# Kernel tuning notes

Measured on AMD Instinct MI355X. Metric: run time of the kernel, lower is better.

The kernel has to match this reference:

```python
import jax, jax.numpy as jnp
import numpy as np

N = 100000
E = 1600000
DIN = 128
HID = 128
EPS = 1e-5


def setup_inputs() -> dict:
    key = jax.random.key(0)
    ks = jax.random.split(key, 16)
    s = lambda i, shape, sc=0.05: jax.random.normal(ks[i], shape, dtype=jnp.float32) * sc
    inp = {
        "x": jax.random.normal(ks[0], (N, DIN), dtype=jnp.float32),
        "edge_index": jax.random.randint(ks[1], (2, E), 0, N, dtype=jnp.int64),
        # layer 1
        "W1": s(2, (DIN, HID)), "b1": jnp.zeros((HID,), jnp.float32),
        "g1": jnp.ones((HID,), jnp.float32), "be1": jnp.zeros((HID,), jnp.float32),
        "m1": s(3, (HID,)), "v1": jax.random.uniform(ks[4], (HID,), jnp.float32) + 0.5,
        # layer 2
        "W2": s(5, (HID, HID)), "b2": jnp.zeros((HID,), jnp.float32),
        "g2": jnp.ones((HID,), jnp.float32), "be2": jnp.zeros((HID,), jnp.float32),
        "m2": s(6, (HID,)), "v2": jax.random.uniform(ks[7], (HID,), jnp.float32) + 0.5,
        # classifier
        "Wc1": s(8, (HID, HID // 2)), "bc1": jnp.zeros((HID // 2,), jnp.float32),
        "Wc2": s(9, (HID // 2, 2)), "bc2": jnp.zeros((2,), jnp.float32),
    }
    return inp


def _gnn_layer(x, W, b, src, dst):
    # linear then scatter-mean of source features onto destinations
    h = x @ W + b                                    # [N, HID]
    msg_sum = jax.ops.segment_sum(h[src], dst, num_segments=N)   # [N, HID]
    cnt = jax.ops.segment_sum(jnp.ones((src.shape[0],), h.dtype), dst, num_segments=N)
    return msg_sum / cnt[:, None]                    # self-loops guarantee cnt >= 1


def _bn(x, g, be, m, v):
    return (x - m) * jax.lax.rsqrt(v + EPS) * g + be


def reference(x, edge_index, W1, b1, g1, be1, m1, v1, W2, b2, g2, be2, m2, v2, Wc1, bc1, Wc2, bc2):
    # add self loops (PyG add_self_loops appends [i, i])
    loop = jnp.arange(N, dtype=edge_index.dtype)
    src = jnp.concatenate([edge_index[0], loop])
    dst = jnp.concatenate([edge_index[1], loop])

    h = _gnn_layer(x, W1, b1, src, dst)
    h = jax.nn.relu(_bn(h, g1, be1, m1, v1))
    h = _gnn_layer(h, W2, b2, src, dst)
    h = jax.nn.relu(_bn(h, g2, be2, m2, v2))

    h = jax.nn.relu(h @ Wc1 + bc1)
    return h @ Wc2 + bc2                              # logits [N, 2]
```

## Files before the change

### kernel.cpp

```cpp
#include <hip/hip_runtime.h>
#include <hip/hip_bf16.h>

#define EPS 1e-5f

using bf16x8 = __attribute__((ext_vector_type(8))) short;
using f32x4  = __attribute__((ext_vector_type(4))) float;

__device__ __forceinline__ void bf16_split(float f, unsigned short& h, unsigned short& l) {
    unsigned u = __float_as_uint(f);
    unsigned hu = (u + 0x8000u) & 0xFFFF0000u;
    float fh = __uint_as_float(hu);
    h = (unsigned short)(hu >> 16);
    float rl = f - fh;
    unsigned ul = __float_as_uint(rl);
    l = (unsigned short)((ul + 0x8000u) >> 16);
}

__global__ __launch_bounds__(256) void k_wprep(const float* __restrict__ W1,
                                               const float* __restrict__ W2,
                                               unsigned short* __restrict__ w1h,
                                               unsigned short* __restrict__ w1l,
                                               unsigned short* __restrict__ w2h,
                                               unsigned short* __restrict__ w2l) {
    int idx = blockIdx.x * 256 + threadIdx.x;
    if (idx >= 32768) return;
    int mtx = idx >> 14;
    int rem = idx & 16383;
    int k = rem >> 7, n = rem & 127;
    float w = mtx ? W2[k * 128 + n] : W1[k * 128 + n];
    unsigned short h, l;
    bf16_split(w, h, l);
    if (mtx) { w2h[n * 128 + k] = h; w2l[n * 128 + k] = l; }
    else     { w1h[n * 128 + k] = h; w1l[n * 128 + k] = l; }
}

__global__ __launch_bounds__(256) void k_histrank(const int* __restrict__ dst,
                                                  int* __restrict__ counts,
                                                  int* __restrict__ rank, int nE) {
    int i = blockIdx.x * 256 + threadIdx.x;
    if (i < nE) {
        int p = atomicAdd(&counts[dst[i]], 1);
        __builtin_nontemporal_store(p, &rank[i]);
    }
}

__global__ __launch_bounds__(256) void k_scan1(const int* __restrict__ counts,
                                               int* __restrict__ bsums, int n) {
    __shared__ int sdata[256];
    int base = blockIdx.x * 2048;
    int t = threadIdx.x;
    int s = 0;
#pragma unroll
    for (int i = 0; i < 8; ++i) {
        int idx = base + t * 8 + i;
        if (idx < n) s += counts[idx];
    }
    sdata[t] = s;
    __syncthreads();
    for (int off = 128; off > 0; off >>= 1) {
        if (t < off) sdata[t] += sdata[t + off];
        __syncthreads();
    }
    if (t == 0) bsums[blockIdx.x] = sdata[0];
}

__global__ __launch_bounds__(64) void k_scan2(int* __restrict__ bsums, int nb) {
    if (threadIdx.x == 0 && blockIdx.x == 0) {
        int acc = 0;
        for (int i = 0; i < nb; ++i) { int v = bsums[i]; bsums[i] = acc; acc += v; }
    }
}

__global__ __launch_bounds__(256) void k_scan3(const int* __restrict__ counts,
                                               const int* __restrict__ bsums,
                                               int* __restrict__ rowstart,
                                               int n, int nE) {
    __shared__ int sth[256];
    int base = blockIdx.x * 2048;
    int t = threadIdx.x;
    int loc[8];
    int s = 0;
#pragma unroll
    for (int i = 0; i < 8; ++i) {
        int idx = base + t * 8 + i;
        loc[i] = s;
        s += (idx < n) ? counts[idx] : 0;
    }
    sth[t] = s;
    __syncthreads();
    for (int off = 1; off < 256; off <<= 1) {
        int tmp = (t >= off) ? sth[t - off] : 0;
        __syncthreads();
        sth[t] += tmp;
        __syncthreads();
    }
    int excl = sth[t] - s + bsums[blockIdx.x];
#pragma unroll
    for (int i = 0; i < 8; ++i) {
        int idx = base + t * 8 + i;
        if (idx < n) rowstart[idx] = excl + loc[i];
    }
    if (blockIdx.x == 0 && t == 0) rowstart[n] = nE;
}

__global__ __launch_bounds__(256) void k_fill3(const int* __restrict__ srci,
                                               const int* __restrict__ dsti,
                                               const int* __restrict__ rank,
                                               const int* __restrict__ rowstart,
                                               int* __restrict__ col, int nE) {
    int e = blockIdx.x * 256 + threadIdx.x;
    if (e < nE) {
        col[rowstart[dsti[e]] + rank[e]] = srci[e];
    }
}

__global__ __launch_bounds__(256) void k_linmf(const float* __restrict__ X,
                                               const unsigned short* __restrict__ WhT,
                                               const unsigned short* __restrict__ WlT,
                                               const float* __restrict__ bias,
                                               float* __restrict__ out, int nRows) {
    __shared__ __align__(16) unsigned short xh[64][136];
    __shared__ __align__(16) unsigned short xl[64][136];
    int row0 = blockIdx.x * 64;
    int tid = threadIdx.x;

    for (int i = tid; i < 64 * 32; i += 256) {
        int r = i >> 5, c4 = (i & 31) << 2;
        float4 v = make_float4(0.f, 0.f, 0.f, 0.f);
        int row = row0 + r;
        if (row < nRows) v = *(const float4*)(X + (size_t)row * 128 + c4);
        unsigned short h0, l0, h1, l1, h2, l2, h3, l3;
        bf16_split(v.x, h0, l0); bf16_split(v.y, h1, l1);
        bf16_split(v.z, h2, l2); bf16_split(v.w, h3, l3);
        xh[r][c4] = h0; xh[r][c4 + 1] = h1; xh[r][c4 + 2] = h2; xh[r][c4 + 3] = h3;
        xl[r][c4] = l0; xl[r][c4 + 1] = l1; xl[r][c4 + 2] = l2; xl[r][c4 + 3] = l3;
    }
    __syncthreads();

    int w = tid >> 6, lane = tid & 63;
    int t16 = lane & 15;
    int kg = lane >> 4;

    f32x4 acc[8];
#pragma unroll
    for (int ct = 0; ct < 8; ++ct) acc[ct] = (f32x4){0.f, 0.f, 0.f, 0.f};

    for (int k0 = 0; k0 < 128; k0 += 32) {
        bf16x8 ah = *(const bf16x8*)&xh[w * 16 + t16][k0 + kg * 8];
        bf16x8 al = *(const bf16x8*)&xl[w * 16 + t16][k0 + kg * 8];
#pragma unroll
        for (int ct = 0; ct < 8; ++ct) {
            size_t boff = (size_t)(ct * 16 + t16) * 128 + k0 + kg * 8;
            bf16x8 bh = *(const bf16x8*)(WhT + boff);
            bf16x8 bl = *(const bf16x8*)(WlT + boff);
            acc[ct] = __builtin_amdgcn_mfma_f32_16x16x32_bf16(ah, bh, acc[ct], 0, 0, 0);
            acc[ct] = __builtin_amdgcn_mfma_f32_16x16x32_bf16(ah, bl, acc[ct], 0, 0, 0);
            acc[ct] = __builtin_amdgcn_mfma_f32_16x16x32_bf16(al, bh, acc[ct], 0, 0, 0);
        }
    }

#pragma unroll
    for (int ct = 0; ct < 8; ++ct) {
        int c = ct * 16 + t16;
        float b = bias[c];
#pragma unroll
        for (int j = 0; j < 4; ++j) {
            int r = row0 + w * 16 + kg * 4 + j;
            if (r < nRows) out[(size_t)r * 128 + c] = acc[ct][j] + b;
        }
    }
}

template <bool FUSE_BN>
__global__ __launch_bounds__(256) void k_gather(const float* __restrict__ src,
                                                const int* __restrict__ rowstart,
                                                const int* __restrict__ col,
                                                const float* __restrict__ g,
                                                const float* __restrict__ be,
                                                const float* __restrict__ m,
                                                const float* __restrict__ v,
                                                float* __restrict__ out, int nRows) {
    int r = blockIdx.x * 4 + (threadIdx.x >> 6);
    if (r >= nRows) return;
    int lane = threadIdx.x & 63;
    int half = lane >> 5;
    int li = lane & 31;
    int d0 = li * 4;
    int s = rowstart[r], e = rowstart[r + 1];
    int deg = e - s;

    float4 acc = make_float4(0.f, 0.f, 0.f, 0.f);
    if (half == 0) acc = *(const float4*)(src + (size_t)r * 128 + d0);

    int nP = deg >> 1;
    int p = 0;
    for (; p + 4 <= nP; p += 4) {
        int jb = s + 2 * p + half;
        int c0i = col[jb], c1i = col[jb + 2], c2i = col[jb + 4], c3i = col[jb + 6];
        float4 t0 = *(const float4*)(src + (size_t)c0i * 128 + d0);
        float4 t1 = *(const float4*)(src + (size_t)c1i * 128 + d0);
        float4 t2 = *(const float4*)(src + (size_t)c2i * 128 + d0);
        float4 t3 = *(const float4*)(src + (size_t)c3i * 128 + d0);
        acc.x += (t0.x + t1.x) + (t2.x + t3.x);
        acc.y += (t0.y + t1.y) + (t2.y + t3.y);
        acc.z += (t0.z + t1.z) + (t2.z + t3.z);
        acc.w += (t0.w + t1.w) + (t2.w + t3.w);
    }
    for (; p < nP; ++p) {
        int ci = col[s + 2 * p + half];
        float4 t = *(const float4*)(src + (size_t)ci * 128 + d0);
        acc.x += t.x; acc.y += t.y; acc.z += t.z; acc.w += t.w;
    }
    if ((deg & 1) && half == 0) {
        int ci = col[e - 1];
        float4 t = *(const float4*)(src + (size_t)ci * 128 + d0);
        acc.x += t.x; acc.y += t.y; acc.z += t.z; acc.w += t.w;
    }

    acc.x += __shfl_xor(acc.x, 32, 64);
    acc.y += __shfl_xor(acc.y, 32, 64);
    acc.z += __shfl_xor(acc.z, 32, 64);
    acc.w += __shfl_xor(acc.w, 32, 64);

    if (half == 0) {
        float rc = 1.0f / (float)(deg + 1);
        float4 o;
        if (FUSE_BN) {
            float4 gv  = *(const float4*)(g + d0);
            float4 bev = *(const float4*)(be + d0);
            float4 mv  = *(const float4*)(m + d0);
            float4 vv  = *(const float4*)(v + d0);
            o.x = fmaxf((acc.x * rc - mv.x) * rsqrtf(vv.x + EPS) * gv.x + bev.x, 0.f);
            o.y = fmaxf((acc.y * rc - mv.y) * rsqrtf(vv.y + EPS) * gv.y + bev.y, 0.f);
            o.z = fmaxf((acc.z * rc - mv.z) * rsqrtf(vv.z + EPS) * gv.z + bev.z, 0.f);
            o.w = fmaxf((acc.w * rc - mv.w) * rsqrtf(vv.w + EPS) * gv.w + bev.w, 0.f);
        } else {
            o.x = acc.x * rc; o.y = acc.y * rc; o.z = acc.z * rc; o.w = acc.w * rc;
        }
        *(float4*)(out + (size_t)r * 128 + d0) = o;
    }
}

__global__ __launch_bounds__(256) void k_final(const float* __restrict__ xin,
                                               const float* __restrict__ Wc1,
                                               const float* __restrict__ bc1,
                                               const float* __restrict__ Wc2,
                                               const float* __restrict__ bc2,
                                               float* __restrict__ out, int nRows) {
    __shared__ float xs[32][132];
    __shared__ float w1s[128][64];
    __shared__ float hs[32][68];
    int row0 = blockIdx.x * 32;
    int tid = threadIdx.x;

    for (int i = tid; i < 2048; i += 256) {
        int kk = i >> 4, c4 = (i & 15) << 2;
        *(float4*)&w1s[kk][c4] = *(const float4*)(Wc1 + kk * 64 + c4);
    }
    for (int i = tid; i < 1024; i += 256) {
        int r = i >> 5, c4 = (i & 31) << 2;
        int row = row0 + r;
        float4 o = make_float4(0.f, 0.f, 0.f, 0.f);
        if (row < nRows) o = *(const float4*)(xin + (size_t)row * 128 + c4);
        *(float4*)&xs[r][c4] = o;
    }
    __syncthreads();

    int cg = tid & 15, rg = tid >> 4;
    int c0 = cg * 4, r0 = rg * 2;
    float acc[2][4];
    float4 bc = *(const float4*)(bc1 + c0);
    acc[0][0] = bc.x; acc[0][1] = bc.y; acc[0][2] = bc.z; acc[0][3] = bc.w;
    acc[1][0] = bc.x; acc[1][1] = bc.y; acc[1][2] = bc.z; acc[1][3] = bc.w;
    for (int k = 0; k < 128; ++k) {
        float4 w4 = *(const float4*)&w1s[k][c0];
        float x0 = xs[r0][k], x1 = xs[r0 + 1][k];
        acc[0][0] = fmaf(x0, w4.x, acc[0][0]);
        acc[0][1] = fmaf(x0, w4.y, acc[0][1]);
        acc[0][2] = fmaf(x0, w4.z, acc[0][2]);
        acc[0][3] = fmaf(x0, w4.w, acc[0][3]);
        acc[1][0] = fmaf(x1, w4.x, acc[1][0]);
        acc[1][1] = fmaf(x1, w4.y, acc[1][1]);
        acc[1][2] = fmaf(x1, w4.z, acc[1][2]);
        acc[1][3] = fmaf(x1, w4.w, acc[1][3]);
    }
    *(float4*)&hs[r0][c0] = make_float4(fmaxf(acc[0][0], 0.f), fmaxf(acc[0][1], 0.f),
                                        fmaxf(acc[0][2], 0.f), fmaxf(acc[0][3], 0.f));
    *(float4*)&hs[r0 + 1][c0] = make_float4(fmaxf(acc[1][0], 0.f), fmaxf(acc[1][1], 0.f),
                                            fmaxf(acc[1][2], 0.f), fmaxf(acc[1][3], 0.f));
    __syncthreads();

    if (tid < 64) {
        int r = tid >> 1, oc = tid & 1;
        float s = bc2[oc];
        for (int c = 0; c < 64; ++c) s = fmaf(hs[r][c], Wc2[c * 2 + oc], s);
        int row = row0 + r;
        if (row < nRows) out[(size_t)row * 2 + oc] = s;
    }
}

extern "C" void kernel_launch(void* const* d_in, const int* in_sizes, int n_in,
                              void* d_out, int out_size, void* d_ws, size_t ws_size,
                              hipStream_t stream) {
    const float* x   = (const float*)d_in[0];
    const int*   ei  = (const int*)d_in[1];
    const float* W1  = (const float*)d_in[2];
    const float* b1  = (const float*)d_in[3];
    const float* g1  = (const float*)d_in[4];
    const float* be1 = (const float*)d_in[5];
    const float* m1  = (const float*)d_in[6];
    const float* v1  = (const float*)d_in[7];
    const float* W2  = (const float*)d_in[8];
    const float* b2  = (const float*)d_in[9];
    const float* g2  = (const float*)d_in[10];
    const float* be2 = (const float*)d_in[11];
    const float* m2  = (const float*)d_in[12];
    const float* v2  = (const float*)d_in[13];
    const float* Wc1 = (const float*)d_in[14];
    const float* bc1 = (const float*)d_in[15];
    const float* Wc2 = (const float*)d_in[16];
    const float* bc2 = (const float*)d_in[17];

    const int N_ = in_sizes[0] / 128;
    const int E_ = in_sizes[1] / 2;
    const int* srci = ei;
    const int* dsti = ei + E_;

    float* A = (float*)d_ws;
    float* B = A + (size_t)N_ * 128;
    int* rank = (int*)B;
    int* counts   = (int*)(B + (size_t)N_ * 128);
    int* rowstart = counts + N_;
    int* bsums    = rowstart + N_ + 1;
    int* col      = bsums + 256;
    uintptr_t wp  = ((uintptr_t)(col + E_) + 63) & ~(uintptr_t)63;
    unsigned short* w1h = (unsigned short*)wp;
    unsigned short* w1l = w1h + 16384;
    unsigned short* w2h = w1l + 16384;
    unsigned short* w2l = w2h + 16384;

    const int nb = (N_ + 2047) / 2048;

    k_wprep<<<128, 256, 0, stream>>>(W1, W2, w1h, w1l, w2h, w2l);

    hipMemsetAsync(counts, 0, (size_t)N_ * sizeof(int), stream);
    k_histrank<<<(E_ + 255) / 256, 256, 0, stream>>>(dsti, counts, rank, E_);
    k_scan1   <<<nb, 256, 0, stream>>>(counts, bsums, N_);
    k_scan2   <<<1, 64, 0, stream>>>(bsums, nb);
    k_scan3   <<<nb, 256, 0, stream>>>(counts, bsums, rowstart, N_, E_);
    k_fill3   <<<(E_ + 255) / 256, 256, 0, stream>>>(srci, dsti, rank, rowstart,
                                                     col, E_);

    k_linmf<<<(N_ + 63) / 64, 256, 0, stream>>>(x, w1h, w1l, b1, A, N_);
    k_gather<true><<<(N_ + 3) / 4, 256, 0, stream>>>(A, rowstart, col,
                                                     g1, be1, m1, v1, B, N_);

    k_linmf<<<(N_ + 63) / 64, 256, 0, stream>>>(B, w2h, w2l, b2, A, N_);
    k_gather<true><<<(N_ + 3) / 4, 256, 0, stream>>>(A, rowstart, col,
                                                     g2, be2, m2, v2, B, N_);

    k_final<<<(N_ + 31) / 32, 256, 0, stream>>>(B, Wc1, bc1, Wc2, bc2,
                                                (float*)d_out, N_);
}
```

Baseline: 652.4 us.

## Aggregate before linear and fuse layer-2 linear with classifier head

Uses linearity of mean aggregation to gather raw features first and then apply the linear layer, with bias, BN and ReLU fused into the MFMA epilogue. The second layer's linear, BN and ReLU are fused with the two-layer classifier head in one kernel that keeps the hidden tile in shared memory. This drops one full N×128 write and read plus a kernel launch. The cost is a heavier head kernel that reads Wc1 from global memory instead of staging it in LDS, and an extra shared-memory round trip.

```diff
diff --git a/kernel.cpp b/kernel.cpp
--- a/kernel.cpp
+++ b/kernel.cpp
@@ -114,71 +114,9 @@
     }
 }
 
-__global__ __launch_bounds__(256) void k_linmf(const float* __restrict__ X,
-                                               const unsigned short* __restrict__ WhT,
-                                               const unsigned short* __restrict__ WlT,
-                                               const float* __restrict__ bias,
-                                               float* __restrict__ out, int nRows) {
-    __shared__ __align__(16) unsigned short xh[64][136];
-    __shared__ __align__(16) unsigned short xl[64][136];
-    int row0 = blockIdx.x * 64;
-    int tid = threadIdx.x;
-
-    for (int i = tid; i < 64 * 32; i += 256) {
-        int r = i >> 5, c4 = (i & 31) << 2;
-        float4 v = make_float4(0.f, 0.f, 0.f, 0.f);
-        int row = row0 + r;
-        if (row < nRows) v = *(const float4*)(X + (size_t)row * 128 + c4);
-        unsigned short h0, l0, h1, l1, h2, l2, h3, l3;
-        bf16_split(v.x, h0, l0); bf16_split(v.y, h1, l1);
-        bf16_split(v.z, h2, l2); bf16_split(v.w, h3, l3);
-        xh[r][c4] = h0; xh[r][c4 + 1] = h1; xh[r][c4 + 2] = h2; xh[r][c4 + 3] = h3;
-        xl[r][c4] = l0; xl[r][c4 + 1] = l1; xl[r][c4 + 2] = l2; xl[r][c4 + 3] = l3;
-    }
-    __syncthreads();
-
-    int w = tid >> 6, lane = tid & 63;
-    int t16 = lane & 15;
-    int kg = lane >> 4;
-
-    f32x4 acc[8];
-#pragma unroll
-    for (int ct = 0; ct < 8; ++ct) acc[ct] = (f32x4){0.f, 0.f, 0.f, 0.f};
-
-    for (int k0 = 0; k0 < 128; k0 += 32) {
-        bf16x8 ah = *(const bf16x8*)&xh[w * 16 + t16][k0 + kg * 8];
-        bf16x8 al = *(const bf16x8*)&xl[w * 16 + t16][k0 + kg * 8];
-#pragma unroll
-        for (int ct = 0; ct < 8; ++ct) {
-            size_t boff = (size_t)(ct * 16 + t16) * 128 + k0 + kg * 8;
-            bf16x8 bh = *(const bf16x8*)(WhT + boff);
-            bf16x8 bl = *(const bf16x8*)(WlT + boff);
-            acc[ct] = __builtin_amdgcn_mfma_f32_16x16x32_bf16(ah, bh, acc[ct], 0, 0, 0);
-            acc[ct] = __builtin_amdgcn_mfma_f32_16x16x32_bf16(ah, bl, acc[ct], 0, 0, 0);
-            acc[ct] = __builtin_amdgcn_mfma_f32_16x16x32_bf16(al, bh, acc[ct], 0, 0, 0);
-        }
-    }
-
-#pragma unroll
-    for (int ct = 0; ct < 8; ++ct) {
-        int c = ct * 16 + t16;
-        float b = bias[c];
-#pragma unroll
-        for (int j = 0; j < 4; ++j) {
-            int r = row0 + w * 16 + kg * 4 + j;
-            if (r < nRows) out[(size_t)r * 128 + c] = acc[ct][j] + b;
-        }
-    }
-}
-
-template <bool FUSE_BN>
 __global__ __launch_bounds__(256) void k_gather(const float* __restrict__ src,
                                                 const int* __restrict__ rowstart,
                                                 const int* __restrict__ col,
-                                                const float* __restrict__ g,
-                                                const float* __restrict__ be,
-                                                const float* __restrict__ m,
-                                                const float* __restrict__ v,
                                                 float* __restrict__ out, int nRows) {
     int r = blockIdx.x * 4 + (threadIdx.x >> 6);
     if (r >= nRows) return;
@@ -224,73 +162,177 @@
 
     if (half == 0) {
         float rc = 1.0f / (float)(deg + 1);
-        float4 o;
-        if (FUSE_BN) {
-            float4 gv  = *(const float4*)(g + d0);
-            float4 bev = *(const float4*)(be + d0);
-            float4 mv  = *(const float4*)(m + d0);
-            float4 vv  = *(const float4*)(v + d0);
-            o.x = fmaxf((acc.x * rc - mv.x) * rsqrtf(vv.x + EPS) * gv.x + bev.x, 0.f);
-            o.y = fmaxf((acc.y * rc - mv.y) * rsqrtf(vv.y + EPS) * gv.y + bev.y, 0.f);
-            o.z = fmaxf((acc.z * rc - mv.z) * rsqrtf(vv.z + EPS) * gv.z + bev.z, 0.f);
-            o.w = fmaxf((acc.w * rc - mv.w) * rsqrtf(vv.w + EPS) * gv.w + bev.w, 0.f);
-        } else {
-            o.x = acc.x * rc; o.y = acc.y * rc; o.z = acc.z * rc; o.w = acc.w * rc;
-        }
+        float4 o = make_float4(acc.x * rc, acc.y * rc, acc.z * rc, acc.w * rc);
         *(float4*)(out + (size_t)r * 128 + d0) = o;
     }
 }
 
-__global__ __launch_bounds__(256) void k_final(const float* __restrict__ xin,
-                                               const float* __restrict__ Wc1,
-                                               const float* __restrict__ bc1,
-                                               const float* __restrict__ Wc2,
-                                               const float* __restrict__ bc2,
-                                               float* __restrict__ out, int nRows) {
-    __shared__ float xs[32][132];
-    __shared__ float w1s[128][64];
-    __shared__ float hs[32][68];
-    int row0 = blockIdx.x * 32;
+__global__ __launch_bounds__(256) void k_lin_bn(const float* __restrict__ X,
+                                                const unsigned short* __restrict__ WhT,
+                                                const unsigned short* __restrict__ WlT,
+                                                const float* __restrict__ bias,
+                                                const float* __restrict__ g,
+                                                const float* __restrict__ be,
+                                                const float* __restrict__ m,
+                                                const float* __restrict__ v,
+                                                float* __restrict__ out, int nRows) {
+    __shared__ __align__(16) unsigned short xh[64][136];
+    __shared__ __align__(16) unsigned short xl[64][136];
+    int row0 = blockIdx.x * 64;
     int tid = threadIdx.x;
 
-    for (int i = tid; i < 2048; i += 256) {
-        int kk = i >> 4, c4 = (i & 15) << 2;
-        *(float4*)&w1s[kk][c4] = *(const float4*)(Wc1 + kk * 64 + c4);
-    }
-    for (int i = tid; i < 1024; i += 256) {
+    for (int i = tid; i < 64 * 32; i += 256) {
         int r = i >> 5, c4 = (i & 31) << 2;
+        float4 vv = make_float4(0.f, 0.f, 0.f, 0.f);
         int row = row0 + r;
-        float4 o = make_float4(0.f, 0.f, 0.f, 0.f);
-        if (row < nRows) o = *(const float4*)(xin + (size_t)row * 128 + c4);
-        *(float4*)&xs[r][c4] = o;
-    }
-    __syncthreads();
-
-    int cg = tid & 15, rg = tid >> 4;
-    int c0 = cg * 4, r0 = rg * 2;
-    float acc[2][4];
-    float4 bc = *(const float4*)(bc1 + c0);
-    acc[0][0] = bc.x; acc[0][1] = bc.y; acc[0][2] = bc.z; acc[0][3] = bc.w;
-    acc[1][0] = bc.x; acc[1][1] = bc.y; acc[1][2] = bc.z; acc[1][3] = bc.w;
-    for (int k = 0; k < 128; ++k) {
-        float4 w4 = *(const float4*)&w1s[k][c0];
-        float x0 = xs[r0][k], x1 = xs[r0 + 1][k];
-        acc[0][0] = fmaf(x0, w4.x, acc[0][0]);
-        acc[0][1] = fmaf(x0, w4.y, acc[0][1]);
-        acc[0][2] = fmaf(x0, w4.z, acc[0][2]);
-        acc[0][3] = fmaf(x0, w4.w, acc[0][3]);
-        acc[1][0] = fmaf(x1, w4.x, acc[1][0]);
-        acc[1][1] = fmaf(x1, w4.y, acc[1][1]);
-        acc[1][2] = fmaf(x1, w4.z, acc[1][2]);
-        acc[1][3] = fmaf(x1, w4.w, acc[1][3]);
-    }
-    *(float4*)&hs[r0][c0] = make_float4(fmaxf(acc[0][0], 0.f), fmaxf(acc[0][1], 0.f),
-                                        fmaxf(acc[0][2], 0.f), fmaxf(acc[0][3], 0.f));
-    *(float4*)&hs[r0 + 1][c0] = make_float4(fmaxf(acc[1][0], 0.f), fmaxf(acc[1][1], 0.f),
-                                            fmaxf(acc[1][2], 0.f), fmaxf(acc[1][3], 0.f));
-    __syncthreads();
-
-    if (tid < 64) {
+        if (row < nRows) vv = *(const float4*)(X + (size_t)row * 128 + c4);
+        unsigned short h0, l0, h1, l1, h2, l2, h3, l3;
+        bf16_split(vv.x, h0, l0); bf16_split(vv.y, h1, l1);
+        bf16_split(vv.z, h2, l2); bf16_split(vv.w, h3, l3);
+        xh[r][c4] = h0; xh[r][c4 + 1] = h1; xh[r][c4 + 2] = h2; xh[r][c4 + 3] = h3;
+        xl[r][c4] = l0; xl[r][c4 + 1] = l1; xl[r][c4 + 2] = l2; xl[r][c4 + 3] = l3;
+    }
+    __syncthreads();
+
+    int w = tid >> 6, lane = tid & 63;
+    int t16 = lane & 15;
+    int kg = lane >> 4;
+
+    f32x4 acc[8];
+#pragma unroll
+    for (int ct = 0; ct < 8; ++ct) acc[ct] = (f32x4){0.f, 0.f, 0.f, 0.f};
+
+    for (int k0 = 0; k0 < 128; k0 += 32) {
+        bf16x8 ah = *(const bf16x8*)&xh[w * 16 + t16][k0 + kg * 8];
+        bf16x8 al = *(const bf16x8*)&xl[w * 16 + t16][k0 + kg * 8];
+#pragma unroll
+        for (int ct = 0; ct < 8; ++ct) {
+            size_t boff = (size_t)(ct * 16 + t16) * 128 + k0 + kg * 8;
+            bf16x8 bh = *(const bf16x8*)(WhT + boff);
+            bf16x8 bl = *(const bf16x8*)(WlT + boff);
+            acc[ct] = __builtin_amdgcn_mfma_f32_16x16x32_bf16(ah, bh, acc[ct], 0, 0, 0);
+            acc[ct] = __builtin_amdgcn_mfma_f32_16x16x32_bf16(ah, bl, acc[ct], 0, 0, 0);
+            acc[ct] = __builtin_amdgcn_mfma_f32_16x16x32_bf16(al, bh, acc[ct], 0, 0, 0);
+        }
+    }
+
+#pragma unroll
+    for (int ct = 0; ct < 8; ++ct) {
+        int c = ct * 16 + t16;
+        float sc = rsqrtf(v[c] + EPS) * g[c];
+        float sh = be[c] - m[c] * sc;
+        float bb = bias[c];
+#pragma unroll
+        for (int j = 0; j < 4; ++j) {
+            int r = row0 + w * 16 + kg * 4 + j;
+            if (r < nRows)
+                out[(size_t)r * 128 + c] = fmaxf((acc[ct][j] + bb) * sc + sh, 0.f);
+        }
+    }
+}
+
+__global__ __launch_bounds__(256) void k_lin2_head(const float* __restrict__ X,
+                                                   const unsigned short* __restrict__ WhT,
+                                                   const unsigned short* __restrict__ WlT,
+                                                   const float* __restrict__ bias,
+                                                   const float* __restrict__ g,
+                                                   const float* __restrict__ be,
+                                                   const float* __restrict__ m,
+                                                   const float* __restrict__ v,
+                                                   const float* __restrict__ Wc1,
+                                                   const float* __restrict__ bc1,
+                                                   const float* __restrict__ Wc2,
+                                                   const float* __restrict__ bc2,
+                                                   float* __restrict__ out, int nRows) {
+    __shared__ __align__(16) char smem[64 * 136 * 2 * 2];
+    __shared__ float hs[64][68];
+    unsigned short (*xh)[136] = (unsigned short (*)[136])smem;
+    unsigned short (*xl)[136] = (unsigned short (*)[136])(smem + 64 * 136 * 2);
+    float (*xs)[132] = (float (*)[132])smem;
+
+    int row0 = blockIdx.x * 64;
+    int tid = threadIdx.x;
+
+    for (int i = tid; i < 64 * 32; i += 256) {
+        int r = i >> 5, c4 = (i & 31) << 2;
+        float4 vv = make_float4(0.f, 0.f, 0.f, 0.f);
+        int row = row0 + r;
+        if (row < nRows) vv = *(const float4*)(X + (size_t)row * 128 + c4);
+        unsigned short h0, l0, h1, l1, h2, l2, h3, l3;
+        bf16_split(vv.x, h0, l0); bf16_split(vv.y, h1, l1);
+        bf16_split(vv.z, h2, l2); bf16_split(vv.w, h3, l3);
+        xh[r][c4] = h0; xh[r][c4 + 1] = h1; xh[r][c4 + 2] = h2; xh[r][c4 + 3] = h3;
+        xl[r][c4] = l0; xl[r][c4 + 1] = l1; xl[r][c4 + 2] = l2; xl[r][c4 + 3] = l3;
+    }
+    __syncthreads();
+
+    int w = tid >> 6, lane = tid & 63;
+    int t16 = lane & 15;
+    int kg = lane >> 4;
+
+    f32x4 acc[8];
+#pragma unroll
+    for (int ct = 0; ct < 8; ++ct) acc[ct] = (f32x4){0.f, 0.f, 0.f, 0.f};
+
+    for (int k0 = 0; k0 < 128; k0 += 32) {
+        bf16x8 ah = *(const bf16x8*)&xh[w * 16 + t16][k0 + kg * 8];
+        bf16x8 al = *(const bf16x8*)&xl[w * 16 + t16][k0 + kg * 8];
+#pragma unroll
+        for (int ct = 0; ct < 8; ++ct) {
+            size_t boff = (size_t)(ct * 16 + t16) * 128 + k0 + kg * 8;
+            bf16x8 bh = *(const bf16x8*)(WhT + boff);
+            bf16x8 bl = *(const bf16x8*)(WlT + boff);
+            acc[ct] = __builtin_amdgcn_mfma_f32_16x16x32_bf16(ah, bh, acc[ct], 0, 0, 0);
+            acc[ct] = __builtin_amdgcn_mfma_f32_16x16x32_bf16(ah, bl, acc[ct], 0, 0, 0);
+            acc[ct] = __builtin_amdgcn_mfma_f32_16x16x32_bf16(al, bh, acc[ct], 0, 0, 0);
+        }
+    }
+    __syncthreads();
+
+#pragma unroll
+    for (int ct = 0; ct < 8; ++ct) {
+        int c = ct * 16 + t16;
+        float sc = rsqrtf(v[c] + EPS) * g[c];
+        float sh = be[c] - m[c] * sc;
+        float bb = bias[c];
+#pragma unroll
+        for (int j = 0; j < 4; ++j) {
+            int lr = w * 16 + kg * 4 + j;
+            xs[lr][c] = fmaxf((acc[ct][j] + bb) * sc + sh, 0.f);
+        }
+    }
+    __syncthreads();
+
+    {
+        int cg = tid & 15, rg = tid >> 4;
+        int c0 = cg * 4, r0 = rg * 4;
+        float a2[4][4];
+        float4 bc = *(const float4*)(bc1 + c0);
+#pragma unroll
+        for (int i = 0; i < 4; ++i) {
+            a2[i][0] = bc.x; a2[i][1] = bc.y; a2[i][2] = bc.z; a2[i][3] = bc.w;
+        }
+        for (int k = 0; k < 128; ++k) {
+            float4 w4 = *(const float4*)(Wc1 + k * 64 + c0);
+#pragma unroll
+            for (int i = 0; i < 4; ++i) {
+                float xk = xs[r0 + i][k];
+                a2[i][0] = fmaf(xk, w4.x, a2[i][0]);
+                a2[i][1] = fmaf(xk, w4.y, a2[i][1]);
+                a2[i][2] = fmaf(xk, w4.z, a2[i][2]);
+                a2[i][3] = fmaf(xk, w4.w, a2[i][3]);
+            }
+        }
+#pragma unroll
+        for (int i = 0; i < 4; ++i) {
+            *(float4*)&hs[r0 + i][c0] =
+                make_float4(fmaxf(a2[i][0], 0.f), fmaxf(a2[i][1], 0.f),
+                            fmaxf(a2[i][2], 0.f), fmaxf(a2[i][3], 0.f));
+        }
+    }
+    __syncthreads();
+
+    if (tid < 128) {
         int r = tid >> 1, oc = tid & 1;
         float s = bc2[oc];
         for (int c = 0; c < 64; ++c) s = fmaf(hs[r][c], Wc2[c * 2 + oc], s);
@@ -351,14 +393,13 @@
     k_fill3   <<<(E_ + 255) / 256, 256, 0, stream>>>(srci, dsti, rank, rowstart,
                                                      col, E_);
 
-    k_linmf<<<(N_ + 63) / 64, 256, 0, stream>>>(x, w1h, w1l, b1, A, N_);
-    k_gather<true><<<(N_ + 3) / 4, 256, 0, stream>>>(A, rowstart, col,
-                                                     g1, be1, m1, v1, B, N_);
-
-    k_linmf<<<(N_ + 63) / 64, 256, 0, stream>>>(B, w2h, w2l, b2, A, N_);
-    k_gather<true><<<(N_ + 3) / 4, 256, 0, stream>>>(A, rowstart, col,
-                                                     g2, be2, m2, v2, B, N_);
-
-    k_final<<<(N_ + 31) / 32, 256, 0, stream>>>(B, Wc1, bc1, Wc2, bc2,
-                                                (float*)d_out, N_);
-}
+    k_gather<<<(N_ + 3) / 4, 256, 0, stream>>>(x, rowstart, col, A, N_);
+    k_lin_bn<<<(N_ + 63) / 64, 256, 0, stream>>>(A, w1h, w1l, b1,
+                                                 g1, be1, m1, v1, B, N_);
+
+    k_gather<<<(N_ + 3) / 4, 256, 0, stream>>>(B, rowstart, col, A, N_);
+    k_lin2_head<<<(N_ + 63) / 64, 256, 0, stream>>>(A, w2h, w2l, b2,
+                                                    g2, be2, m2, v2,
+                                                    Wc1, bc1, Wc2, bc2,
+                                                    (float*)d_out, N_);
+}
```

Result: faster. 634.2 us (-2.8%).
